# Performance work log

Measured on AMD Instinct MI355X. Metric: run time of the kernel, lower is better.

## Reference

```python
import jax, jax.numpy as jnp
import numpy as np

B, C, T, N = 8, 128, 12, 4096
E_HALF = 131072
EPS = 1e-5


def _linear_params(key, fan_in, fan_out):
    kw, kb = jax.random.split(key)
    bound = 1.0 / np.sqrt(fan_in)
    W = jax.random.uniform(kw, (fan_in, fan_out), jnp.float32, -bound, bound)
    b = jax.random.uniform(kb, (fan_out,), jnp.float32, -bound, bound)
    return W, b


def setup_inputs() -> dict:
    key = jax.random.key(0)
    ks = jax.random.split(key, 10)
    h_in = jax.random.normal(ks[0], (B, C, T, N), jnp.float32)
    # symmetric edge list: random pairs + reverses + self loops
    u = jax.random.randint(ks[1], (E_HALF,), 0, N, jnp.int32)
    v = jax.random.randint(ks[2], (E_HALF,), 0, N, jnp.int32)
    loops = jnp.arange(N, dtype=jnp.int32)
    row = jnp.concatenate([u, v, loops])
    col = jnp.concatenate([v, u, loops])
    edge_index = jnp.stack([row, col])  # [2, E]
    Wq, bq = _linear_params(ks[3], C, C)
    Wk, bk = _linear_params(ks[4], C, C)
    Wv, bv = _linear_params(ks[5], C, C)
    W1, b1 = _linear_params(ks[6], 2 * C, 4 * C)
    W2, b2 = _linear_params(ks[7], 4 * C, C)
    W3, b3 = _linear_params(ks[8], C, 1)
    return dict(h_in=h_in, edge_index=edge_index, Wq=Wq, bq=bq, Wk=Wk, bk=bk,
                Wv=Wv, bv=bv, W1=W1, b1=b1, W2=W2, b2=b2, W3=W3, b3=b3)


def _masked_instance_norm(x, mask_f):
    # stats over the non-self-loop edges only (matching torch, where the MLP
    # only sees edge_index[:, non_self_loop_mask])
    cnt = mask_f.sum()
    mean = (x * mask_f).sum(0) / cnt
    var = (((x - mean) ** 2) * mask_f).sum(0) / cnt
    return (x - mean) / jnp.sqrt(var + EPS)


def _forward(h_in, edge_index, Wq, bq, Wk, bk, Wv, bv, W1, b1, W2, b2, W3, b3):
    # ---- TemporalAttention ----
    x = jnp.transpose(h_in, (0, 3, 2, 1))  # [B, N, T, C]
    q = x @ Wq + bq
    k = x @ Wk + bk
    v = x @ Wv + bv
    scores = jnp.einsum('bntc,bnsc->bnts', q, k) / (C ** 0.5)
    attn = jax.nn.softmax(scores, axis=-1)
    weighted = jnp.einsum('bnts,bnsc->bntc', attn, v)
    emb = weighted.sum(axis=2)          # [B, N, C]
    emb_mean = emb.mean(axis=0)         # [N, C]

    # ---- ExtractorMLP on non-self-loop edges ----
    row, col = edge_index[0], edge_index[1]
    self_loop = row == col
    mask_f = (~self_loop).astype(emb_mean.dtype)[:, None]  # [E, 1]
    f12 = jnp.concatenate([emb_mean[row], emb_mean[col]], axis=-1)  # [E, 2C]
    h = jax.nn.relu(_masked_instance_norm(f12 @ W1 + b1, mask_f))
    h = jax.nn.relu(_masked_instance_norm(h @ W2 + b2, mask_f))
    logits = h @ W3 + b3                 # [E, 1]

    # concrete_sample, eval mode (deterministic)
    att = jax.nn.sigmoid(logits)
    all_att = jnp.where(self_loop[:, None], 1.0, att)  # [E, 1]

    # ---- transpose + reorder_like: match each edge with its reverse ----
    M = jnp.max(edge_index) + 1
    fwd_key = row * M + col
    rev_key = col * M + row
    order = jnp.argsort(fwd_key)
    pos = jnp.searchsorted(fwd_key[order], rev_key)
    perm = order[pos]                    # index of reverse edge
    edge_att = (all_att + all_att[perm]) * 0.5
    return edge_att


def reference(h_in, edge_index, Wq, bq, Wk, bk, Wv, bv, W1, b1, W2, b2, W3, b3):
    return _forward(h_in, edge_index, Wq, bq, Wk, bk, Wv, bv, W1, b1, W2, b2, W3, b3)
```

## Files before the change

### kernel.cpp

```cpp
#include <hip/hip_runtime.h>
#include <hip/hip_bf16.h>

#define CC     128
#define TT     12
#define NNODE  4096
#define NE     266240
#define EHALF  131072
#define F1     512
#define EPS    1e-5f
#define RSQRTC 0.08838834764831845f
#define EB     64
#define NBLKG  4160
#define NF2A   65
#define ST     40

#define O_XWM   0ull
#define O_W1S   524288ull
#define O_W2S   524800ull
#define O_ICNT  525312ull
#define O_CNT   525440ull
#define O_T     529536ull
#define O_S     529664ull
#define O_GTB   546048ull
#define O_W0B   554240ull
#define O_WC1   554304ull
#define O_WC2   619840ull
#define O_B1C   685376ull
#define O_M1    685888ull
#define O_IS1   686400ull
#define O_M2    686912ull
#define O_IS2   687040ull
#define O_CROSS 687168ull
#define O_W2T   687680ull
#define O_PB    720448ull
#define O_QB    1769024ull
#define O_ALLA  2817600ull
#define O_PART  3083840ull
#define O_PART2 4148800ull
#define O_Z2    4165440ull

typedef __attribute__((ext_vector_type(8))) short bf16x8;
typedef __attribute__((ext_vector_type(4))) float f32x4;

__device__ inline float bfbits2f(unsigned int v) { return __uint_as_float(v << 16); }
__device__ inline unsigned short f2bf(float x) {
  union { __hip_bfloat16 h; unsigned short u; } cv;
  cv.h = __float2bfloat16(x);
  return cv.u;
}
__device__ inline float f4get(const float4& v, int k) {
  return k == 0 ? v.x : k == 1 ? v.y : k == 2 ? v.z : v.w;
}

__global__ void k_pre(const float* __restrict__ Wq, const float* __restrict__ bq,
                      const float* __restrict__ Wk,
                      unsigned short* __restrict__ Gtb, unsigned short* __restrict__ w0b) {
  int i = blockIdx.x, j = threadIdx.x;
  float acc = 0.f;
  for (int co = 0; co < CC; ++co) acc = fmaf(Wq[i*CC+co], Wk[j*CC+co], acc);
  Gtb[j*CC + i] = f2bf(acc);
  if (j == 0) {
    float a = 0.f;
    for (int co = 0; co < CC; ++co) a = fmaf(Wk[i*CC+co], bq[co], a);
    w0b[i] = f2bf(a);
  }
}

__global__ __launch_bounds__(256) void k_prew(const float* __restrict__ Wv,
    const float* __restrict__ bv, const float* __restrict__ W1, const float* __restrict__ b1,
    float* __restrict__ Wc1, float* __restrict__ Wc2, float* __restrict__ b1c) {
  __shared__ float wvr[CC];
  const int c = blockIdx.x, tid = threadIdx.x;
  if (tid < CC) wvr[tid] = Wv[(size_t)c*CC + tid];
  __syncthreads();
  for (int h = 0; h < 2; ++h) {
    int f = h*256 + tid;
    float a1 = 0.f, a2 = 0.f;
    for (int j = 0; j < CC; ++j) {
      float wv = wvr[j];
      a1 = fmaf(wv, W1[(size_t)j*F1 + f], a1);
      a2 = fmaf(wv, W1[(size_t)(CC + j)*F1 + f], a2);
    }
    Wc1[(size_t)c*F1 + f] = a1;
    Wc2[(size_t)c*F1 + f] = a2;
  }
  if (c == 0) {
    for (int h = 0; h < 2; ++h) {
      int f = h*256 + tid;
      float s = b1[f];
      for (int j = 0; j < CC; ++j)
        s = fmaf(12.f*bv[j], W1[(size_t)j*F1 + f] + W1[(size_t)(CC + j)*F1 + f], s);
      b1c[f] = s;
    }
  }
}

__global__ void k_w2t(const float* __restrict__ W2, unsigned short* __restrict__ W2T) {
  int n = blockIdx.x;
  for (int k = threadIdx.x; k < F1; k += 256)
    W2T[(size_t)n*F1 + k] = f2bf(W2[(size_t)k*CC + n]);
}

__global__ __launch_bounds__(256) void k_hist(const int* __restrict__ row,
    const int* __restrict__ col, int* __restrict__ cnt, int* __restrict__ icnt) {
  __shared__ int h[NNODE];
  const int tid = threadIdx.x;
  for (int i = tid; i < NNODE; i += 256) h[i] = 0;
  __syncthreads();
  int lc = 0;
  const int base = blockIdx.x << 12;
  for (int i = tid; i < 4096; i += 256) {
    int e = base + i;
    int r = row[e], c = col[e];
    if (r != c) { atomicAdd(&h[r], 1); ++lc; }
  }
  #pragma unroll
  for (int d = 1; d < 64; d <<= 1) lc += __shfl_xor(lc, d);
  __syncthreads();
  for (int i = tid; i < NNODE; i += 256) { int v = h[i]; if (v) atomicAdd(&cnt[i], v); }
  if ((tid & 63) == 0) atomicAdd(icnt, lc);
}

__global__ __launch_bounds__(256, 8) void k_attn(
    const float* __restrict__ h_in,
    const unsigned short* __restrict__ Gtb,
    const unsigned short* __restrict__ w0b,
    float* __restrict__ xwm) {
  __shared__ unsigned short xs[48*128];
  __shared__ unsigned short ys[48*128];
  __shared__ float dsv[48];
  const int tid = threadIdx.x;
  const int bid = ((blockIdx.x & 7) << 10) | (blockIdx.x >> 3);
  const int b  = bid >> 10;
  const int n0 = (bid & 1023) << 2;

  const int w = tid >> 6, lane = tid & 63;
  const int l15 = lane & 15, l4 = lane >> 4;

  {
    const int c2 = tid & 63;
    const float* g0 = h_in + (((size_t)b*CC + 2*c2)*TT + w)*NNODE + n0;
    float4 av[3], bv[3];
    #pragma unroll
    for (int it = 0; it < 3; ++it) {
      av[it] = *(const float4*)(g0 + (size_t)(4*it)*NNODE);
      bv[it] = *(const float4*)(g0 + (size_t)(TT + 4*it)*NNODE);
    }
    unsigned wp = *(const unsigned*)(w0b + 2*c2);
    float w0f0 = bfbits2f(wp & 0xffffu), w0f1 = bfbits2f(wp >> 16);
    #pragma unroll
    for (int it = 0; it < 3; ++it) {
      int t = w + it*4;
      #pragma unroll
      for (int i = 0; i < 4; ++i) {
        float xa = f4get(av[it], i);
        float xb = f4get(bv[it], i);
        int r = i*TT + t;
        unsigned byte = ((unsigned)r << 8) + (((unsigned)(c2*4)) ^ (((unsigned)(r & 7)) << 4));
        *(unsigned*)((char*)xs + byte) = (unsigned)f2bf(xa) | ((unsigned)f2bf(xb) << 16);
        float dd = fmaf(xa, w0f0, xb * w0f1);
        #pragma unroll
        for (int d = 1; d < 64; d <<= 1) dd += __shfl_xor(dd, d);
        if (lane == 0) dsv[r] = dd;
      }
    }
  }
  __syncthreads();

  {
    f32x4 acc[2][3];
    #pragma unroll
    for (int mt = 0; mt < 2; ++mt)
      #pragma unroll
      for (int nt = 0; nt < 3; ++nt) acc[mt][nt] = (f32x4){0.f,0.f,0.f,0.f};

    #pragma unroll
    for (int kt = 0; kt < 4; ++kt) {
      bf16x8 gf[2];
      #pragma unroll
      for (int mt = 0; mt < 2; ++mt)
        gf[mt] = *(const bf16x8*)(Gtb + (size_t)((w<<5) + (mt<<4) + l15)*CC + (kt<<5) + (l4<<3));
      bf16x8 bfr[3];
      #pragma unroll
      for (int nt = 0; nt < 3; ++nt) {
        int rr = nt*16 + l15;
        unsigned byte = ((unsigned)rr << 8) +
                        (((unsigned)((kt<<6) + (l4<<4))) ^ (((unsigned)(rr & 7)) << 4));
        bfr[nt] = *(const bf16x8*)((const char*)xs + byte);
      }
      #pragma unroll
      for (int mt = 0; mt < 2; ++mt)
        #pragma unroll
        for (int nt = 0; nt < 3; ++nt)
          acc[mt][nt] = __builtin_amdgcn_mfma_f32_16x16x32_bf16(gf[mt], bfr[nt], acc[mt][nt], 0, 0, 0);
    }
    #pragma unroll
    for (int mt = 0; mt < 2; ++mt)
      #pragma unroll
      for (int nt = 0; nt < 3; ++nt) {
        int rr = nt*16 + l15;
        ushort4 v;
        v.x = f2bf(acc[mt][nt][0]); v.y = f2bf(acc[mt][nt][1]);
        v.z = f2bf(acc[mt][nt][2]); v.w = f2bf(acc[mt][nt][3]);
        unsigned cb = (unsigned)((w<<6) + (mt<<5) + (l4<<3));
        unsigned byte = ((unsigned)rr << 8) + (cb ^ (((unsigned)(rr & 7)) << 4));
        *(ushort4*)((char*)ys + byte) = v;
      }
  }
  __syncthreads();

  {
    const int rb = w*TT;
    const bool sval = (l15 < TT);
    const int rr = rb + (sval ? l15 : 0);
    f32x4 sa = (f32x4){0.f,0.f,0.f,0.f};
    #pragma unroll
    for (int kt = 0; kt < 4; ++kt) {
      unsigned byte = ((unsigned)rr << 8) +
                      (((unsigned)((kt<<6) + (l4<<4))) ^ (((unsigned)(rr & 7)) << 4));
      bf16x8 afr = *(const bf16x8*)((const char*)ys + byte);
      bf16x8 bfr = *(const bf16x8*)((const char*)xs + byte);
      sa = __builtin_amdgcn_mfma_f32_16x16x32_bf16(afr, bfr, sa, 0, 0, 0);
    }
    float dv = dsv[rr];
    float p[4];
    #pragma unroll
    for (int r = 0; r < 4; ++r) {
      float t1 = sval ? (sa[r] + dv) * RSQRTC : -1e30f;
      float m = t1;
      m = fmaxf(m, __shfl_xor(m, 1));
      m = fmaxf(m, __shfl_xor(m, 2));
      m = fmaxf(m, __shfl_xor(m, 4));
      m = fmaxf(m, __shfl_xor(m, 8));
      float e = exp2f((t1 - m) * 1.4426950408889634f);
      float s = e;
      s += __shfl_xor(s, 1);
      s += __shfl_xor(s, 2);
      s += __shfl_xor(s, 4);
      s += __shfl_xor(s, 8);
      p[r] = e / s;
    }
    float wpart = (l4 < 3) ? (p[0] + p[1] + p[2] + p[3]) : 0.f;
    wpart += __shfl_xor(wpart, 16);
    wpart += __shfl_xor(wpart, 32);
    float xw0 = 0.f, xw1 = 0.f;
    #pragma unroll
    for (int s = 0; s < TT; ++s) {
      float wv = __shfl(wpart, s);
      int r2 = rb + s;
      unsigned byte = ((unsigned)r2 << 8) +
                      (((unsigned)(lane << 2)) ^ (((unsigned)(r2 & 7)) << 4));
      unsigned xp = *(const unsigned*)((const char*)xs + byte);
      xw0 = fmaf(wv, bfbits2f(xp & 0xffffu), xw0);
      xw1 = fmaf(wv, bfbits2f(xp >> 16), xw1);
    }
    unsafeAtomicAdd(&xwm[(size_t)(n0 + w)*CC + (lane << 1)],     xw0 * 0.125f);
    unsafeAtomicAdd(&xwm[(size_t)(n0 + w)*CC + (lane << 1) + 1], xw1 * 0.125f);
  }
}

__global__ __launch_bounds__(256) void k_t(const float* __restrict__ xwm,
    const int* __restrict__ cnt, float* __restrict__ t) {
  __shared__ float ts[256];
  const int tid = threadIdx.x;
  const int f = tid & 127;
  const int n0 = blockIdx.x << 7;
  float s = 0.f;
  for (int i = (tid >> 7); i < 128; i += 2) {
    int n = n0 + i;
    s = fmaf((float)cnt[n], xwm[(size_t)n*CC + f], s);
  }
  ts[tid] = s;
  __syncthreads();
  if (tid < 128) unsafeAtomicAdd(&t[f], ts[tid] + ts[tid + 128]);
}

__global__ __launch_bounds__(256) void k_S(const float* __restrict__ xwm,
    const int* __restrict__ row, const int* __restrict__ col, float* __restrict__ S) {
  __shared__ unsigned short XT[128*ST];
  __shared__ unsigned short YT[128*ST];
  const int tid = threadIdx.x;
  const int w = tid >> 6, lane = tid & 63, l15 = lane & 15, l4 = lane >> 4;
  const int j = tid & 31, fi = tid >> 5;
  const int f0 = fi << 4;
  f32x4 acc[2][8];
  #pragma unroll
  for (int mt = 0; mt < 2; ++mt)
    #pragma unroll
    for (int nt = 0; nt < 8; ++nt) acc[mt][nt] = (f32x4){0.f,0.f,0.f,0.f};

  const int ebase = blockIdx.x << 9;
  for (int bt = 0; bt < 16; ++bt) {
    const int e = ebase + (bt << 5) + j;
    const int r = row[e], c = col[e];
    const bool msk = (r != c);
    const float* xr = xwm + (size_t)r*CC + f0;
    const float* xc = xwm + (size_t)c*CC + f0;
    float4 xv[4], yv[4];
    #pragma unroll
    for (int u = 0; u < 4; ++u) { xv[u] = *(const float4*)(xr + 4*u); yv[u] = *(const float4*)(xc + 4*u); }
    __syncthreads();
    #pragma unroll
    for (int u = 0; u < 16; ++u) {
      float xvv = f4get(xv[u >> 2], u & 3);
      float yvv = f4get(yv[u >> 2], u & 3);
      XT[(f0+u)*ST + j] = f2bf(xvv);
      YT[(f0+u)*ST + j] = msk ? f2bf(yvv) : (unsigned short)0;
    }
    __syncthreads();
    bf16x8 af[2];
    #pragma unroll
    for (int mt = 0; mt < 2; ++mt)
      af[mt] = *(const bf16x8*)&XT[((((w<<1)+mt)<<4) + l15)*ST + (l4<<3)];
    #pragma unroll
    for (int nt = 0; nt < 8; ++nt) {
      bf16x8 bf_ = *(const bf16x8*)&YT[(((nt<<4) + l15))*ST + (l4<<3)];
      acc[0][nt] = __builtin_amdgcn_mfma_f32_16x16x32_bf16(af[0], bf_, acc[0][nt], 0, 0, 0);
      acc[1][nt] = __builtin_amdgcn_mfma_f32_16x16x32_bf16(af[1], bf_, acc[1][nt], 0, 0, 0);
    }
  }
  #pragma unroll
  for (int mt = 0; mt < 2; ++mt)
    #pragma unroll
    for (int nt = 0; nt < 8; ++nt)
      #pragma unroll
      for (int reg = 0; reg < 4; ++reg) {
        int a = (((w<<1)+mt)<<4) + (l4<<2) + reg;
        int b = (nt<<4) + l15;
        unsafeAtomicAdd(&S[a*128 + b], acc[mt][nt][reg]);
      }
}

__global__ __launch_bounds__(128) void k_cross(const float* __restrict__ S,
    const float* __restrict__ Wc1, const float* __restrict__ Wc2,
    const float* __restrict__ b1c, const float* __restrict__ t,
    float* __restrict__ cross) {
  __shared__ float w2c[128];
  __shared__ float red[128], red2[128];
  const int f = blockIdx.x, a = threadIdx.x;
  w2c[a] = Wc2[(size_t)a*F1 + f];
  __syncthreads();
  float v = 0.f;
  const float* Sr = S + a*128;
  for (int b = 0; b < 128; b += 4) {
    float4 sv = *(const float4*)(Sr + b);
    v = fmaf(sv.x, w2c[b],   v); v = fmaf(sv.y, w2c[b+1], v);
    v = fmaf(sv.z, w2c[b+2], v); v = fmaf(sv.w, w2c[b+3], v);
  }
  float pa = Wc1[(size_t)a*F1 + f] * v;
  float ta = t[a] * w2c[a];
  #pragma unroll
  for (int d = 1; d < 64; d <<= 1) { pa += __shfl_xor(pa, d); ta += __shfl_xor(ta, d); }
  red[a] = pa; red2[a] = ta;
  __syncthreads();
  if (a == 0) cross[f] = red[0] + red[64] + b1c[f]*(red2[0] + red2[64]);
}

__global__ __launch_bounds__(256) void k_pq(const float* __restrict__ xwm,
    const float* __restrict__ Wc1, const float* __restrict__ Wc2,
    const float* __restrict__ b1c, const int* __restrict__ cnt,
    unsigned short* __restrict__ Pb, unsigned short* __restrict__ Qb,
    float* __restrict__ w1, float* __restrict__ w2) {
  __shared__ float em[4][CC];
  const int tid = threadIdx.x;
  const int n0 = blockIdx.x << 2;
  for (int i = tid; i < 4*CC; i += 256)
    em[i >> 7][i & 127] = xwm[(size_t)(n0 + (i >> 7))*CC + (i & 127)];
  __syncthreads();
  float ws[2] = {0.f, 0.f}, qs[2] = {0.f, 0.f};
  for (int nn = 0; nn < 4; ++nn) {
    const float cw = (float)cnt[n0 + nn];
    for (int half = 0; half < 2; ++half) {
      int f = half*256 + tid;
      float ap = b1c[f], aq = 0.f;
      for (int c = 0; c < CC; ++c) {
        float e = em[nn][c];
        ap = fmaf(e, Wc1[(size_t)c*F1 + f], ap);
        aq = fmaf(e, Wc2[(size_t)c*F1 + f], aq);
      }
      unsigned short pu = f2bf(ap), qu = f2bf(aq);
      Pb[(size_t)(n0+nn)*F1 + f] = pu;
      Qb[(size_t)(n0+nn)*F1 + f] = qu;
      float pf = bfbits2f(pu), qf = bfbits2f(qu);
      ws[half] = fmaf(cw, pf + qf, ws[half]);
      qs[half] = fmaf(cw, pf*pf + qf*qf, qs[half]);
    }
  }
  unsafeAtomicAdd(&w1[tid],       ws[0]);
  unsafeAtomicAdd(&w1[tid + 256], ws[1]);
  unsafeAtomicAdd(&w2[tid],       qs[0]);
  unsafeAtomicAdd(&w2[tid + 256], qs[1]);
}

__global__ void k_fin1(const float* __restrict__ w1, const float* __restrict__ w2,
                       const float* __restrict__ cross, const int* __restrict__ icnt,
                       float* __restrict__ m1, float* __restrict__ is1) {
  int f = threadIdx.x;
  float cnt = (float)(*icnt);
  float m = w1[f] / cnt;
  m1[f] = m;
  is1[f] = rsqrtf((w2[f] + 2.f*cross[f]) / cnt - m*m + EPS);
}

__global__ __launch_bounds__(512, 4) void k_gemm(const unsigned short* __restrict__ Pb,
    const unsigned short* __restrict__ Qb, const int* __restrict__ row,
    const int* __restrict__ col,
    const float* __restrict__ m1, const float* __restrict__ is1,
    const unsigned short* __restrict__ W2T, const float* __restrict__ b2,
    unsigned short* __restrict__ z2, float* __restrict__ part) {
  __shared__ unsigned short h1s[EB*F1];
  __shared__ float m1s[F1], is1s[F1];
  __shared__ int rS[EB], cS[EB]; __shared__ float mk[EB];
  __shared__ float cstat[256];
  const int tid = threadIdx.x;
  const int bid = blockIdx.x;
  const int e0 = bid * EB;
  const int w = tid >> 6, lane = tid & 63;
  const int wn0 = w << 4;
  const int l15 = lane & 15, l4 = lane >> 4;
  if (tid < EB) {
    int r = row[e0+tid], c = col[e0+tid];
    rS[tid] = r; cS[tid] = c; mk[tid] = (r != c) ? 1.f : 0.f;
  }
  for (int i = tid; i < F1; i += 512) { m1s[i] = m1[i]; is1s[i] = is1[i]; }
  __syncthreads();

  {
    const int j = tid >> 3;
    const unsigned short* pr = Pb + (size_t)rS[j]*F1;
    const unsigned short* qr = Qb + (size_t)cS[j]*F1;
    const int sw = (j & 7) << 4;
    const unsigned rowb = (unsigned)j << 10;
    #pragma unroll
    for (int half = 0; half < 2; ++half) {
      uint4 pv[4], qv[4];
      #pragma unroll
      for (int u = 0; u < 4; ++u) {
        int k0 = (((tid & 7) + ((half*4 + u) << 3)) << 3);
        pv[u] = *(const uint4*)(pr + k0);
        qv[u] = *(const uint4*)(qr + k0);
      }
      #pragma unroll
      for (int u = 0; u < 4; ++u) {
        int k0 = (((tid & 7) + ((half*4 + u) << 3)) << 3);
        unsigned out[4];
        #pragma unroll
        for (int q = 0; q < 4; ++q) {
          unsigned pu = (&pv[u].x)[q], qu = (&qv[u].x)[q];
          int k = k0 + 2*q;
          float2 mm = *(const float2*)&m1s[k];
          float2 ii = *(const float2*)&is1s[k];
          float za = bfbits2f(pu & 0xffffu) + bfbits2f(qu & 0xffffu);
          float zb = bfbits2f(pu >> 16)     + bfbits2f(qu >> 16);
          float ha = fmaxf((za - mm.x)*ii.x, 0.f);
          float hb = fmaxf((zb - mm.y)*ii.y, 0.f);
          out[q] = (unsigned)f2bf(ha) | ((unsigned)f2bf(hb) << 16);
        }
        unsigned byte = rowb + (((unsigned)(k0 << 1)) ^ sw);
        *(uint4*)((char*)h1s + byte) = make_uint4(out[0], out[1], out[2], out[3]);
      }
    }
  }
  __syncthreads();

  f32x4 acc[4];
  #pragma unroll
  for (int a = 0; a < 4; ++a) acc[a] = (f32x4){0.f,0.f,0.f,0.f};

  const unsigned short* w2p = W2T + (size_t)(wn0 + l15)*F1 + (l4 << 3);
  #pragma unroll
  for (int kt = 0; kt < 16; ++kt) {
    bf16x8 bfr = *(const bf16x8*)(w2p + (kt << 5));
    bf16x8 afr[4];
    #pragma unroll
    for (int mt = 0; mt < 4; ++mt) {
      int j = (mt << 4) + l15;
      unsigned byte = ((unsigned)j << 10) + (((unsigned)(kt*64 + l4*16)) ^ ((j & 7) << 4));
      afr[mt] = *(const bf16x8*)((const char*)h1s + byte);
    }
    #pragma unroll
    for (int mt = 0; mt < 4; ++mt)
      acc[mt] = __builtin_amdgcn_mfma_f32_16x16x32_bf16(afr[mt], bfr, acc[mt], 0, 0, 0);
  }
  __syncthreads();

  float* z2s = (float*)&h1s[0];
  const int colg = wn0 + l15;
  {
    float bb = b2[colg];
    float sloc = 0.f, qloc = 0.f;
    #pragma unroll
    for (int mt = 0; mt < 4; ++mt) {
      f32x4 v = acc[mt];
      #pragma unroll
      for (int reg = 0; reg < 4; ++reg) {
        int j = (mt << 4) + (l4 << 2) + reg;
        float z = v[reg] + bb;
        float m = mk[j];
        sloc = fmaf(m, z, sloc);
        qloc = fmaf(m*z, z, qloc);
        z2s[j*132 + colg] = z;
      }
    }
    sloc += __shfl_xor(sloc, 16); sloc += __shfl_xor(sloc, 32);
    qloc += __shfl_xor(qloc, 16); qloc += __shfl_xor(qloc, 32);
    if (l4 == 0) { cstat[colg] = sloc; cstat[128 + colg] = qloc; }
  }
  __syncthreads();

  #pragma unroll
  for (int p = 0; p < 2; ++p) {
    int idx = (p << 12) + (tid << 3);
    int j = idx >> 7, c = idx & 127;
    const float* src = &z2s[j*132 + c];
    float4 v0 = *(const float4*)src;
    float4 v1 = *(const float4*)(src + 4);
    uint4 o;
    o.x = (unsigned)f2bf(v0.x) | ((unsigned)f2bf(v0.y) << 16);
    o.y = (unsigned)f2bf(v0.z) | ((unsigned)f2bf(v0.w) << 16);
    o.z = (unsigned)f2bf(v1.x) | ((unsigned)f2bf(v1.y) << 16);
    o.w = (unsigned)f2bf(v1.z) | ((unsigned)f2bf(v1.w) << 16);
    *(uint4*)(z2 + (size_t)e0*CC + idx) = o;
  }
  if (tid < 256) part[(size_t)bid*256 + tid] = cstat[tid];
}

__global__ __launch_bounds__(256) void k_fin2a(const float* __restrict__ part,
                                               float* __restrict__ part2) {
  const int g = blockIdx.x, tid = threadIdx.x;
  float s = 0.f;
  #pragma unroll 4
  for (int r = 0; r < 64; ++r)
    s += part[(size_t)(g*64 + r)*256 + tid];
  part2[(size_t)g*256 + tid] = s;
}

__global__ __launch_bounds__(256) void k_fin2b(const float* __restrict__ part2,
    const int* __restrict__ icnt, float* __restrict__ m2, float* __restrict__ is2) {
  __shared__ float red[256];
  const int tid = threadIdx.x;
  float s = 0.f;
  for (int g = 0; g < NF2A; ++g) s += part2[(size_t)g*256 + tid];
  red[tid] = s;
  __syncthreads();
  if (tid < 128) {
    float cnt = (float)(*icnt);
    float m = red[tid] / cnt;
    m2[tid] = m;
    is2[tid] = rsqrtf(red[128 + tid]/cnt - m*m + EPS);
  }
}

__global__ __launch_bounds__(256) void k_score(const unsigned short* __restrict__ z2,
    const int* __restrict__ row, const int* __restrict__ col,
    const float* __restrict__ m2, const float* __restrict__ is2,
    const float* __restrict__ W3, const float* __restrict__ b3,
    float* __restrict__ all_att) {
  __shared__ float zt[64][129];
  const int tid = threadIdx.x;
  const int e0 = blockIdx.x << 6;
  const uint4* src = reinterpret_cast<const uint4*>(z2 + (size_t)e0*CC);
  for (int i = tid; i < 64*CC/8; i += 256) {
    uint4 v = src[i];
    int flat = i*8;
    int j = flat >> 7, k = flat & 127;
    zt[j][k+0] = bfbits2f(v.x & 0xffffu); zt[j][k+1] = bfbits2f(v.x >> 16);
    zt[j][k+2] = bfbits2f(v.y & 0xffffu); zt[j][k+3] = bfbits2f(v.y >> 16);
    zt[j][k+4] = bfbits2f(v.z & 0xffffu); zt[j][k+5] = bfbits2f(v.z >> 16);
    zt[j][k+6] = bfbits2f(v.w & 0xffffu); zt[j][k+7] = bfbits2f(v.w >> 16);
  }
  __syncthreads();
  const int j = tid >> 2, q = tid & 3;
  float a = 0.f;
  for (int k = q*32; k < q*32 + 32; ++k)
    a = fmaf(fmaxf((zt[j][k] - m2[k])*is2[k], 0.f), W3[k], a);
  a += __shfl_xor(a, 1, 4);
  a += __shfl_xor(a, 2, 4);
  if (q == 0) {
    int e = e0 + j;
    int r = row[e], c = col[e];
    float att;
    if (r == c) att = 1.f;
    else        att = 1.f / (1.f + expf(-(a + b3[0])));
    all_att[e] = att;
  }
}

__global__ __launch_bounds__(256) void k_out(const float* __restrict__ all_att,
    float* __restrict__ out) {
  int e = blockIdx.x*256 + threadIdx.x;
  int p = (e < EHALF) ? (e + EHALF) : (e < 2*EHALF ? e - EHALF : e);
  out[e] = 0.5f * (all_att[e] + all_att[p]);
}

extern "C" void kernel_launch(void* const* d_in, const int* in_sizes, int n_in,
                              void* d_out, int out_size, void* d_ws, size_t ws_size,
                              hipStream_t stream) {
  const float* h_in = (const float*)d_in[0];
  const int*   ei   = (const int*)d_in[1];
  const float* Wq = (const float*)d_in[2];
  const float* bq = (const float*)d_in[3];
  const float* Wk = (const float*)d_in[4];
  const float* bk = (const float*)d_in[5];  (void)bk;
  const float* Wv = (const float*)d_in[6];
  const float* bv = (const float*)d_in[7];
  const float* W1 = (const float*)d_in[8];
  const float* b1 = (const float*)d_in[9];
  const float* W2 = (const float*)d_in[10];
  const float* b2 = (const float*)d_in[11];
  const float* W3 = (const float*)d_in[12];
  const float* b3 = (const float*)d_in[13];
  float* ws = (float*)d_ws;
  float* out = (float*)d_out;
  const int* row = ei;
  const int* col = ei + NE;

  hipMemsetAsync(ws, 0, 546048ull * 4ull, stream);

  k_pre<<<128, 128, 0, stream>>>(Wq, bq, Wk,
                                 (unsigned short*)(ws+O_GTB), (unsigned short*)(ws+O_W0B));
  k_prew<<<128, 256, 0, stream>>>(Wv, bv, W1, b1, ws+O_WC1, ws+O_WC2, ws+O_B1C);
  k_w2t<<<128, 256, 0, stream>>>(W2, (unsigned short*)(ws+O_W2T));
  k_hist<<<64, 256, 0, stream>>>(row, col, (int*)(ws+O_CNT), (int*)(ws+O_ICNT));
  k_attn<<<8192, 256, 0, stream>>>(h_in, (const unsigned short*)(ws+O_GTB),
                                   (const unsigned short*)(ws+O_W0B), ws+O_XWM);
  k_t<<<32, 256, 0, stream>>>(ws+O_XWM, (const int*)(ws+O_CNT), ws+O_T);
  k_S<<<512, 256, 0, stream>>>(ws+O_XWM, row, col, ws+O_S);
  k_pq<<<1024, 256, 0, stream>>>(ws+O_XWM, ws+O_WC1, ws+O_WC2, ws+O_B1C,
                                 (const int*)(ws+O_CNT),
                                 (unsigned short*)(ws+O_PB), (unsigned short*)(ws+O_QB),
                                 ws+O_W1S, ws+O_W2S);
  k_cross<<<512, 128, 0, stream>>>(ws+O_S, ws+O_WC1, ws+O_WC2, ws+O_B1C, ws+O_T,
                                   ws+O_CROSS);
  k_fin1<<<1, 512, 0, stream>>>(ws+O_W1S, ws+O_W2S, ws+O_CROSS,
                                (const int*)(ws+O_ICNT), ws+O_M1, ws+O_IS1);
  k_gemm<<<NBLKG, 512, 0, stream>>>((const unsigned short*)(ws+O_PB),
                                    (const unsigned short*)(ws+O_QB), row, col,
                                    ws+O_M1, ws+O_IS1,
                                    (const unsigned short*)(ws+O_W2T), b2,
                                    (unsigned short*)(ws+O_Z2), ws+O_PART);
  k_fin2a<<<NF2A, 256, 0, stream>>>(ws+O_PART, ws+O_PART2);
  k_fin2b<<<1, 256, 0, stream>>>(ws+O_PART2, (const int*)(ws+O_ICNT), ws+O_M2, ws+O_IS2);
  k_score<<<4160, 256, 0, stream>>>((const unsigned short*)(ws+O_Z2), row, col,
                                    ws+O_M2, ws+O_IS2, W3, b3, ws+O_ALLA);
  k_out<<<1040, 256, 0, stream>>>(ws+O_ALLA, out);
}
```

Baseline: 504.2 us.

## Prescale P/Q by norm stats per node and shrink GEMM edge tile for occupancy

```diff
diff --git a/kernel.cpp b/kernel.cpp
--- a/kernel.cpp
+++ b/kernel.cpp
@@ -9,9 +9,9 @@
 #define F1     512
 #define EPS    1e-5f
 #define RSQRTC 0.08838834764831845f
-#define EB     64
-#define NBLKG  4160
-#define NF2A   65
+#define EBG    48
+#define NBLKG2 5547
+#define NF2B   87
 #define ST     40
 
 #define O_XWM   0ull
@@ -36,8 +36,8 @@
 #define O_QB    1769024ull
 #define O_ALLA  2817600ull
 #define O_PART  3083840ull
-#define O_PART2 4148800ull
-#define O_Z2    4165440ull
+#define O_PART2 4503872ull
+#define O_Z2    4526144ull
 
 typedef __attribute__((ext_vector_type(8))) short bf16x8;
 typedef __attribute__((ext_vector_type(4))) float f32x4;
@@ -402,84 +402,101 @@
   is1[f] = rsqrtf((w2[f] + 2.f*cross[f]) / cnt - m*m + EPS);
 }
 
-__global__ __launch_bounds__(512, 4) void k_gemm(const unsigned short* __restrict__ Pb,
+__global__ __launch_bounds__(256) void k_scale(unsigned short* __restrict__ Pb,
+    unsigned short* __restrict__ Qb, const float* __restrict__ m1,
+    const float* __restrict__ is1) {
+  const int idx = blockIdx.x*256 + threadIdx.x;
+  const int f0 = (idx & 63) << 3;
+  uint4 p = ((const uint4*)Pb)[idx];
+  uint4 q = ((const uint4*)Qb)[idx];
+  uint4 po, pq;
+  unsigned* pw = &po.x; unsigned* qw = &pq.x;
+  #pragma unroll
+  for (int u = 0; u < 4; ++u) {
+    int k = f0 + 2*u;
+    float2 mm = *(const float2*)&m1[k];
+    float2 ii = *(const float2*)&is1[k];
+    unsigned pu = (&p.x)[u], qu = (&q.x)[u];
+    float pa = bfbits2f(pu & 0xffffu) * ii.x;
+    float pb = bfbits2f(pu >> 16)     * ii.y;
+    float qa = (bfbits2f(qu & 0xffffu) - mm.x) * ii.x;
+    float qb = (bfbits2f(qu >> 16)     - mm.y) * ii.y;
+    pw[u] = (unsigned)f2bf(pa) | ((unsigned)f2bf(pb) << 16);
+    qw[u] = (unsigned)f2bf(qa) | ((unsigned)f2bf(qb) << 16);
+  }
+  ((uint4*)Pb)[idx] = po;
+  ((uint4*)Qb)[idx] = pq;
+}
+
+__global__ __launch_bounds__(512, 6) void k_gemm(const unsigned short* __restrict__ Pb,
     const unsigned short* __restrict__ Qb, const int* __restrict__ row,
     const int* __restrict__ col,
-    const float* __restrict__ m1, const float* __restrict__ is1,
     const unsigned short* __restrict__ W2T, const float* __restrict__ b2,
     unsigned short* __restrict__ z2, float* __restrict__ part) {
-  __shared__ unsigned short h1s[EB*F1];
-  __shared__ float m1s[F1], is1s[F1];
-  __shared__ int rS[EB], cS[EB]; __shared__ float mk[EB];
+  __shared__ unsigned short h1s[EBG*F1];
+  __shared__ int rS[EBG], cS[EBG]; __shared__ float mk[EBG];
   __shared__ float cstat[256];
   const int tid = threadIdx.x;
   const int bid = blockIdx.x;
-  const int e0 = bid * EB;
+  const int e0 = bid * EBG;
   const int w = tid >> 6, lane = tid & 63;
   const int wn0 = w << 4;
   const int l15 = lane & 15, l4 = lane >> 4;
-  if (tid < EB) {
-    int r = row[e0+tid], c = col[e0+tid];
-    rS[tid] = r; cS[tid] = c; mk[tid] = (r != c) ? 1.f : 0.f;
-  }
-  for (int i = tid; i < F1; i += 512) { m1s[i] = m1[i]; is1s[i] = is1[i]; }
-  __syncthreads();
-
-  {
-    const int j = tid >> 3;
-    const unsigned short* pr = Pb + (size_t)rS[j]*F1;
-    const unsigned short* qr = Qb + (size_t)cS[j]*F1;
-    const int sw = (j & 7) << 4;
-    const unsigned rowb = (unsigned)j << 10;
-    #pragma unroll
-    for (int half = 0; half < 2; ++half) {
-      uint4 pv[4], qv[4];
-      #pragma unroll
-      for (int u = 0; u < 4; ++u) {
-        int k0 = (((tid & 7) + ((half*4 + u) << 3)) << 3);
-        pv[u] = *(const uint4*)(pr + k0);
-        qv[u] = *(const uint4*)(qr + k0);
-      }
-      #pragma unroll
-      for (int u = 0; u < 4; ++u) {
-        int k0 = (((tid & 7) + ((half*4 + u) << 3)) << 3);
-        unsigned out[4];
-        #pragma unroll
-        for (int q = 0; q < 4; ++q) {
-          unsigned pu = (&pv[u].x)[q], qu = (&qv[u].x)[q];
-          int k = k0 + 2*q;
-          float2 mm = *(const float2*)&m1s[k];
-          float2 ii = *(const float2*)&is1s[k];
-          float za = bfbits2f(pu & 0xffffu) + bfbits2f(qu & 0xffffu);
-          float zb = bfbits2f(pu >> 16)     + bfbits2f(qu >> 16);
-          float ha = fmaxf((za - mm.x)*ii.x, 0.f);
-          float hb = fmaxf((zb - mm.y)*ii.y, 0.f);
-          out[q] = (unsigned)f2bf(ha) | ((unsigned)f2bf(hb) << 16);
-        }
-        unsigned byte = rowb + (((unsigned)(k0 << 1)) ^ sw);
-        *(uint4*)((char*)h1s + byte) = make_uint4(out[0], out[1], out[2], out[3]);
-      }
-    }
-  }
-  __syncthreads();
-
-  f32x4 acc[4];
-  #pragma unroll
-  for (int a = 0; a < 4; ++a) acc[a] = (f32x4){0.f,0.f,0.f,0.f};
+  if (tid < EBG) {
+    int e = e0 + tid;
+    bool valid = e < NE;
+    int r = valid ? row[e] : 0, c = valid ? col[e] : 0;
+    rS[tid] = r; cS[tid] = c; mk[tid] = (valid && r != c) ? 1.f : 0.f;
+  }
+  __syncthreads();
+
+  #pragma unroll
+  for (int rr = 0; rr < 2; ++rr) {
+    int jj[3], cc[3];
+    #pragma unroll
+    for (int s = 0; s < 3; ++s) {
+      int i = tid + ((rr*3 + s) << 9);
+      jj[s] = i >> 6; cc[s] = i & 63;
+    }
+    uint4 pv[3], qv[3];
+    #pragma unroll
+    for (int s = 0; s < 3; ++s) pv[s] = *(const uint4*)(Pb + (size_t)rS[jj[s]]*F1 + (cc[s] << 3));
+    #pragma unroll
+    for (int s = 0; s < 3; ++s) qv[s] = *(const uint4*)(Qb + (size_t)cS[jj[s]]*F1 + (cc[s] << 3));
+    #pragma unroll
+    for (int s = 0; s < 3; ++s) {
+      unsigned out[4];
+      #pragma unroll
+      for (int q = 0; q < 4; ++q) {
+        unsigned pu = (&pv[s].x)[q], qu = (&qv[s].x)[q];
+        float ha = fmaxf(bfbits2f(pu & 0xffffu) + bfbits2f(qu & 0xffffu), 0.f);
+        float hb = fmaxf(bfbits2f(pu >> 16)     + bfbits2f(qu >> 16),     0.f);
+        out[q] = (unsigned)f2bf(ha) | ((unsigned)f2bf(hb) << 16);
+      }
+      unsigned byte = ((unsigned)jj[s] << 10) +
+                      (((unsigned)(cc[s] << 4)) ^ (((unsigned)(jj[s] & 7)) << 4));
+      *(uint4*)((char*)h1s + byte) = make_uint4(out[0], out[1], out[2], out[3]);
+    }
+  }
+  __syncthreads();
+
+  f32x4 acc[3];
+  #pragma unroll
+  for (int a = 0; a < 3; ++a) acc[a] = (f32x4){0.f,0.f,0.f,0.f};
 
   const unsigned short* w2p = W2T + (size_t)(wn0 + l15)*F1 + (l4 << 3);
   #pragma unroll
   for (int kt = 0; kt < 16; ++kt) {
     bf16x8 bfr = *(const bf16x8*)(w2p + (kt << 5));
-    bf16x8 afr[4];
-    #pragma unroll
-    for (int mt = 0; mt < 4; ++mt) {
+    bf16x8 afr[3];
+    #pragma unroll
+    for (int mt = 0; mt < 3; ++mt) {
       int j = (mt << 4) + l15;
       unsigned byte = ((unsigned)j << 10) + (((unsigned)(kt*64 + l4*16)) ^ ((j & 7) << 4));
       afr[mt] = *(const bf16x8*)((const char*)h1s + byte);
     }
     #pragma unroll
-    for (int mt = 0; mt < 4; ++mt)
+    for (int mt = 0; mt < 3; ++mt)
       acc[mt] = __builtin_amdgcn_mfma_f32_16x16x32_bf16(afr[mt], bfr, acc[mt], 0, 0, 0);
   }
   __syncthreads();
@@ -490,7 +507,7 @@
     float bb = b2[colg];
     float sloc = 0.f, qloc = 0.f;
     #pragma unroll
-    for (int mt = 0; mt < 4; ++mt) {
+    for (int mt = 0; mt < 3; ++mt) {
       f32x4 v = acc[mt];
       #pragma unroll
       for (int reg = 0; reg < 4; ++reg) {
@@ -511,16 +528,20 @@
   #pragma unroll
   for (int p = 0; p < 2; ++p) {
     int idx = (p << 12) + (tid << 3);
-    int j = idx >> 7, c = idx & 127;
-    const float* src = &z2s[j*132 + c];
-    float4 v0 = *(const float4*)src;
-    float4 v1 = *(const float4*)(src + 4);
-    uint4 o;
-    o.x = (unsigned)f2bf(v0.x) | ((unsigned)f2bf(v0.y) << 16);
-    o.y = (unsigned)f2bf(v0.z) | ((unsigned)f2bf(v0.w) << 16);
-    o.z = (unsigned)f2bf(v1.x) | ((unsigned)f2bf(v1.y) << 16);
-    o.w = (unsigned)f2bf(v1.z) | ((unsigned)f2bf(v1.w) << 16);
-    *(uint4*)(z2 + (size_t)e0*CC + idx) = o;
+    if (idx < EBG*CC) {
+      int j = idx >> 7, c = idx & 127;
+      if (e0 + j < NE) {
+        const float* src = &z2s[j*132 + c];
+        float4 v0 = *(const float4*)src;
+        float4 v1 = *(const float4*)(src + 4);
+        uint4 o;
+        o.x = (unsigned)f2bf(v0.x) | ((unsigned)f2bf(v0.y) << 16);
+        o.y = (unsigned)f2bf(v0.z) | ((unsigned)f2bf(v0.w) << 16);
+        o.z = (unsigned)f2bf(v1.x) | ((unsigned)f2bf(v1.y) << 16);
+        o.w = (unsigned)f2bf(v1.z) | ((unsigned)f2bf(v1.w) << 16);
+        *(uint4*)(z2 + (size_t)e0*CC + idx) = o;
+      }
+    }
   }
   if (tid < 256) part[(size_t)bid*256 + tid] = cstat[tid];
 }
@@ -529,9 +550,10 @@
                                                float* __restrict__ part2) {
   const int g = blockIdx.x, tid = threadIdx.x;
   float s = 0.f;
-  #pragma unroll 4
-  for (int r = 0; r < 64; ++r)
-    s += part[(size_t)(g*64 + r)*256 + tid];
+  for (int r = 0; r < 64; ++r) {
+    int b = g*64 + r;
+    if (b < NBLKG2) s += part[(size_t)b*256 + tid];
+  }
   part2[(size_t)g*256 + tid] = s;
 }
 
@@ -540,7 +562,7 @@
   __shared__ float red[256];
   const int tid = threadIdx.x;
   float s = 0.f;
-  for (int g = 0; g < NF2A; ++g) s += part2[(size_t)g*256 + tid];
+  for (int g = 0; g < NF2B; ++g) s += part2[(size_t)g*256 + tid];
   red[tid] = s;
   __syncthreads();
   if (tid < 128) {
@@ -634,12 +656,13 @@
                                    ws+O_CROSS);
   k_fin1<<<1, 512, 0, stream>>>(ws+O_W1S, ws+O_W2S, ws+O_CROSS,
                                 (const int*)(ws+O_ICNT), ws+O_M1, ws+O_IS1);
-  k_gemm<<<NBLKG, 512, 0, stream>>>((const unsigned short*)(ws+O_PB),
-                                    (const unsigned short*)(ws+O_QB), row, col,
-                                    ws+O_M1, ws+O_IS1,
-                                    (const unsigned short*)(ws+O_W2T), b2,
-                                    (unsigned short*)(ws+O_Z2), ws+O_PART);
-  k_fin2a<<<NF2A, 256, 0, stream>>>(ws+O_PART, ws+O_PART2);
+  k_scale<<<1024, 256, 0, stream>>>((unsigned short*)(ws+O_PB),
+                                    (unsigned short*)(ws+O_QB), ws+O_M1, ws+O_IS1);
+  k_gemm<<<NBLKG2, 512, 0, stream>>>((const unsigned short*)(ws+O_PB),
+                                     (const unsigned short*)(ws+O_QB), row, col,
+                                     (const unsigned short*)(ws+O_W2T), b2,
+                                     (unsigned short*)(ws+O_Z2), ws+O_PART);
+  k_fin2a<<<NF2B, 256, 0, stream>>>(ws+O_PART, ws+O_PART2);
   k_fin2b<<<1, 256, 0, stream>>>(ws+O_PART2, (const int*)(ws+O_ICNT), ws+O_M2, ws+O_IS2);
   k_score<<<4160, 256, 0, stream>>>((const unsigned short*)(ws+O_Z2), row, col,
                                     ws+O_M2, ws+O_IS2, W3, b3, ws+O_ALLA);
```

After: 515.6 us. +2.3%, slower.
